# Optimization experiments

Measured on AMD Instinct MI355X. Metric: run time of the kernel, lower is better.

The kernel has to match this reference:

```python
import jax, jax.numpy as jnp
import numpy as np
import math

IN_C, OUT_C, KH, KW = 128, 128, 3, 3
GROUPS_NUM, NUM_W = 8, 8
STRIDE, PAD, DIL = 1, 1, 1
BETA = 1.0


def setup_inputs() -> dict:
    key = jax.random.key(0)
    ks = jax.random.split(key, 6)
    B, H, W = 8, 56, 56
    n = IN_C * KH * KW
    bound = math.sqrt(6.0 / n)  # reset_parameters bound for weight templates
    inputs = jax.random.normal(ks[0], (B, IN_C, H, W), jnp.float32)
    mask = jax.random.randint(ks[1], (B, H, W), 0, GROUPS_NUM)
    Alpha = jax.random.uniform(ks[2], (B, GROUPS_NUM, H, W), jnp.float32)
    weight_templates = jax.random.uniform(ks[3], (OUT_C * IN_C * KH * KW, NUM_W), jnp.float32, -bound, bound)
    routing_w = jax.random.normal(ks[4], (GROUPS_NUM * NUM_W, IN_C), jnp.float32) * 0.01
    routing_b = jnp.zeros((GROUPS_NUM * NUM_W,), jnp.float32)
    bias = jnp.zeros((OUT_C,), jnp.float32)
    return dict(inputs=inputs, mask=mask, Alpha=Alpha, weight_templates=weight_templates,
                routing_w=routing_w, routing_b=routing_b, bias=bias, use_alpha=1)


def _unfold(x):
    # torch F.unfold-compatible im2col: [B, C*KH*KW, Ho, Wo], channel-major feature order
    return jax.lax.conv_general_dilated_patches(
        x, (KH, KW), (STRIDE, STRIDE), [(PAD, PAD), (PAD, PAD)],
        rhs_dilation=(DIL, DIL), dimension_numbers=('NCHW', 'OIHW', 'NCHW'))


def reference(inputs, mask, Alpha, weight_templates, routing_w, routing_b, bias, use_alpha):
    B, C, H, W = inputs.shape
    K = IN_C * KH * KW
    # SE-style routing: GAP -> fc -> scaled sigmoid (alpha=1.0 in source)
    x_se = inputs.reshape(B, C, -1).mean(-1)                              # [B, C]
    x_se = 2.0 * jax.nn.sigmoid(x_se @ routing_w.T + routing_b) / NUM_W   # [B, G*num_W]
    # blend weight templates: F.linear(x_se.reshape(-1,num_W), weight)
    w = x_se.reshape(B * GROUPS_NUM, NUM_W) @ weight_templates.T          # [B*G, O*K]
    w = w.reshape(B, GROUPS_NUM, OUT_C, K).transpose(0, 2, 3, 1)          # [B, O, K, G]
    patches = _unfold(inputs)                                             # [B, K, Ho, Wo]
    # per-group convolution outputs, then per-pixel group routing
    y = jnp.einsum('bokg,bkhw->boghw', w, patches)                        # [B, O, G, Ho, Wo]
    if use_alpha:
        probs = jax.nn.softmax(BETA * Alpha, axis=1)                      # soft routing [B, G, Ho, Wo]
    else:
        probs = jax.nn.one_hot(mask, GROUPS_NUM, axis=1, dtype=y.dtype)   # hard per-pixel group select
    out = jnp.einsum('boghw,bghw->bohw', y, probs)
    return out + bias.reshape(1, -1, 1, 1)
```

## Files before the change

### kernel.cpp

```cpp
#include <hip/hip_runtime.h>
#include <stdint.h>

#define IN_C   128
#define OUT_C  128
#define KTOT   1152
#define NG     8
#define NW     8
#define NB     8
#define HH     56
#define WWID   56
#define NPIX   3136
#define PPAD   3200
#define MTOT   1024
#define HALO   58
#define HPIX   (HALO*HALO)


typedef __attribute__((ext_vector_type(8))) short short8;
typedef __attribute__((ext_vector_type(8))) unsigned short ushort8;
typedef __attribute__((ext_vector_type(4))) float f32x4;
typedef __attribute__((ext_vector_type(16))) float f32x16;

__device__ __forceinline__ unsigned short f2bf(float f) {
    unsigned u = __float_as_uint(f);
    u += 0x7FFF + ((u >> 16) & 1);
    return (unsigned short)(u >> 16);
}

__device__ __forceinline__ void cp16(const unsigned short* g, unsigned short* l) {
    __builtin_amdgcn_global_load_lds(
        (const __attribute__((address_space(1))) unsigned int*)g,
        (__attribute__((address_space(3))) unsigned int*)l,
        16, 0, 0);
}

__global__ __launch_bounds__(256) void prep_kernel(const float* __restrict__ in,
                                                   const float* __restrict__ T,
                                                   float* __restrict__ xse,
                                                   unsigned short* __restrict__ Apack,
                                                   unsigned short* __restrict__ Xt) {
    __shared__ __align__(16) unsigned char smem[32768];
    const int blk = blockIdx.x;
    const int t = threadIdx.x;

    if (blk < 1024) {
        const float* src = in + (size_t)blk * NPIX;
        float s = 0.f;
        for (int i = t; i < NPIX / 4; i += 256) {
            float4 v = ((const float4*)src)[i];
            s += v.x + v.y + v.z + v.w;
        }
        #pragma unroll
        for (int off = 32; off; off >>= 1) s += __shfl_down(s, off);
        float* ws4 = (float*)smem;
        if ((t & 63) == 0) ws4[t >> 6] = s;
        __syncthreads();
        if (t == 0)
            xse[blk] = (ws4[0] + ws4[1] + ws4[2] + ws4[3]) * (1.0f / (float)NPIX);
        return;
    }
    if (blk < 1152) {
        unsigned short* lh = (unsigned short*)smem;
        const int o = blk - 1024;
        const float* To = T + (size_t)o * 9216;
        #pragma unroll
        for (int it = 0; it < 9; it++) {
            const int f = it * 256 + t;
            const float4 v = ((const float4*)To)[f];
            ushort4 h;
            h.x = f2bf(v.x); h.y = f2bf(v.y); h.z = f2bf(v.z); h.w = f2bf(v.w);
            *(ushort4*)&lh[f * 4] = h;
        }
        __syncthreads();
        #pragma unroll
        for (int it = 0; it < 5; it++) {
            const int ch = it * 256 + t;
            if (ch < 1152) {
                const int j = ch & 7, kc = ch >> 3;
                const int s = kc >> 4, c0 = (kc & 15) << 3;
                const int stg = s * 4 + ((c0 >> 5) & 3);
                const int khb = (c0 >> 4) & 1;
                const int hib = (c0 >> 3) & 1;
                ushort8 v;
                #pragma unroll
                for (int i = 0; i < 8; i++)
                    v[i] = lh[((c0 + i) * 9 + s) * 8 + j];
                const size_t off = ((((size_t)(o >> 2) * 36 + stg) * 2 + khb) * 64
                                    + hib * 32 + (o & 3) * 8 + j) * 8;
                *(ushort8*)&Apack[off] = v;
            }
        }
        return;
    }
    unsigned short* tile = (unsigned short*)smem;
    const int idx = blk - 1152;
    const int yt = idx % 28;
    const int b  = idx / 28;
    const int y0 = yt * 2;

    #pragma unroll
    for (int it = 0; it < 14; it++) {
        const int f = it * 256 + t;
        const int c = f / 28;
        const int rem = f - c * 28;
        const int y = rem / 14;
        const int x4 = rem - y * 14;
        const float4 v = *(const float4*)(in + ((size_t)(b * IN_C + c)) * NPIX
                                          + (y0 + y) * WWID + x4 * 4);
        unsigned short bf0 = f2bf(v.x), bf1 = f2bf(v.y), bf2 = f2bf(v.z), bf3 = f2bf(v.w);
        const int ppb = (y * WWID + x4 * 4) ^ (((c >> 3) & 15) << 2);
        uint2 pk;
        pk.x = (unsigned)bf0 | ((unsigned)bf1 << 16);
        pk.y = (unsigned)bf2 | ((unsigned)bf3 << 16);
        *(uint2*)&tile[c * 128 + ppb] = pk;
    }
    __syncthreads();

    #pragma unroll
    for (int it = 0; it < 7; it++) {
        const int ch = it * 256 + t;
        const int oct = ch & 15;
        const int pp = ch >> 4;
        const int sw = oct << 2;
        ushort8 v;
        #pragma unroll
        for (int i = 0; i < 8; i++)
            v[i] = tile[(oct * 8 + i) * 128 + (pp ^ sw)];
        const int y2 = (pp >= WWID) ? 1 : 0;
        const int xg = pp - y2 * WWID;
        const size_t hp = (size_t)b * HPIX + (y0 + y2 + 1) * HALO + (xg + 1);
        *(ushort8*)&Xt[hp * 128 + oct * 8] = v;
    }

    if (t < 64) {
        const int pi = t >> 4, oct = t & 15;
        const int yy = y0 + 1 + (pi >> 1);
        const int xx = (pi & 1) * 57;
        *(ushort8*)&Xt[((size_t)b * HPIX + yy * HALO + xx) * 128 + oct * 8] =
            (ushort8){0, 0, 0, 0, 0, 0, 0, 0};
    }
    if (yt == 0 || yt == 27) {
        const int yy = (yt == 0) ? 0 : 57;
        #pragma unroll
        for (int it = 0; it < 4; it++) {
            const int ch = it * 256 + t;
            if (ch < 928) {
                const int xx = ch >> 4, oct = ch & 15;
                *(ushort8*)&Xt[((size_t)b * HPIX + yy * HALO + xx) * 128 + oct * 8] =
                    (ushort8){0, 0, 0, 0, 0, 0, 0, 0};
            }
        }
    }
}

__global__ __launch_bounds__(256) void s_kernel(const float* __restrict__ Alpha,
                                                const int* __restrict__ mask,
                                                const float* __restrict__ xse,
                                                const float* __restrict__ rw,
                                                const float* __restrict__ rb,
                                                const int* __restrict__ use_alpha,
                                                float* __restrict__ Sws) {
    const int b = blockIdx.y;
    const int t = threadIdx.x;
    const int p = blockIdx.x * 256 + t;
    __shared__ float xs[IN_C];
    __shared__ float rsh[64];
    if (t < IN_C) xs[t] = xse[b * IN_C + t];
    __syncthreads();
    if (t < 64) {
        float acc = rb[t];
        #pragma unroll 8
        for (int c = 0; c < IN_C; c++) acc += xs[c] * rw[t * IN_C + c];
        rsh[t] = 0.25f / (1.0f + expf(-acc));
    }
    __syncthreads();
    if (p >= PPAD) return;
    float sj[8] = {0, 0, 0, 0, 0, 0, 0, 0};
    if (p < NPIX) {
        float pr[8];
        if (use_alpha[0]) {
            float a[8], m = -1e30f;
            #pragma unroll
            for (int g = 0; g < 8; g++) {
                a[g] = Alpha[((size_t)(b * NG + g)) * NPIX + p];
                m = fmaxf(m, a[g]);
            }
            float sum = 0.f;
            #pragma unroll
            for (int g = 0; g < 8; g++) { pr[g] = expf(a[g] - m); sum += pr[g]; }
            float inv = 1.f / sum;
            #pragma unroll
            for (int g = 0; g < 8; g++) pr[g] *= inv;
        } else {
            int mg = mask[(size_t)b * NPIX + p];
            #pragma unroll
            for (int g = 0; g < 8; g++) pr[g] = (g == mg) ? 1.f : 0.f;
        }
        #pragma unroll
        for (int g = 0; g < 8; g++)
            #pragma unroll
            for (int j = 0; j < 8; j++) sj[j] += pr[g] * rsh[g * 8 + j];
    }
    float* dst = Sws + ((size_t)b * PPAD + p) * 8;
    *(f32x4*)dst = (f32x4){sj[0], sj[1], sj[2], sj[3]};
    *(f32x4*)(dst + 4) = (f32x4){sj[4], sj[5], sj[6], sj[7]};
}

__global__ __launch_bounds__(256) void gemm_kernel(const unsigned short* __restrict__ Apack,
                                                   const unsigned short* __restrict__ Xt,
                                                   const float* __restrict__ Sws,
                                                   const float* __restrict__ bias,
                                                   float* __restrict__ out) {
    __shared__ __align__(16) unsigned short Bsh[4][512 * 8];
    const int tid = threadIdx.x;
    const int wv = tid >> 6, ln = tid & 63;
    const int u  = ln & 31, hi = ln >> 5;
    const int wrow = wv >> 1, wcol = wv & 1;

    const int lid = blockIdx.x;
    const int b   = lid & 7;
    const int sl  = lid >> 3;
    const int mt  = sl & 7;
    const int nt  = sl >> 3;

    f32x16 acc[2][2];
    #pragma unroll
    for (int i = 0; i < 2; i++)
        #pragma unroll
        for (int j = 0; j < 2; j++)
            #pragma unroll
            for (int e = 0; e < 16; e++) acc[i][j][e] = 0.f;

    const int js = tid & 3;
    const int r0 = tid >> 2,  q0 = js ^ (r0 & 3) ^ ((r0 >> 2) & 3);
    const int r1 = r0 + 64,   q1 = js ^ (r1 & 3) ^ ((r1 >> 2) & 3);
    const int p0 = min(nt * 128 + r0, NPIX - 1);
    const int p1 = min(nt * 128 + r1, NPIX - 1);
    const int y0p = p0 / WWID, x0p = p0 - y0p * WWID;
    const int y1p = p1 / WWID, x1p = p1 - y1p * WWID;
    const unsigned short* gb0 = Xt + ((size_t)b * HPIX + y0p * HALO + x0p) * 128 + q0 * 8;
    const unsigned short* gb1 = Xt + ((size_t)b * HPIX + y1p * HALO + x1p) * 128 + q1 * 8;
    unsigned short* lbA[4];
    #pragma unroll
    for (int i = 0; i < 4; i++) lbA[i] = &Bsh[i][(wv * 64) * 8];

    const unsigned short* gawB[2];
    #pragma unroll
    for (int tm = 0; tm < 2; tm++) {
        const int m32 = mt * 4 + wrow * 2 + tm;
        gawB[tm] = Apack + (size_t)m32 * 36864 + ln * 8;
    }

    const int jbase = hi ^ (u & 3) ^ ((u >> 2) & 3);
    int boffL[2][2];
    #pragma unroll
    for (int tn = 0; tn < 2; tn++)
        #pragma unroll
        for (int kh = 0; kh < 2; kh++) {
            const int row = wcol * 64 + tn * 32 + u;
            boffL[tn][kh] = (row * 4 + (jbase ^ (kh << 1))) * 8;
        }

#define ALOAD(Ad, st_) { _Pragma("unroll")                                    \
        for (int tm_ = 0; tm_ < 2; tm_++) { _Pragma("unroll")                 \
            for (int kh_ = 0; kh_ < 2; kh_++)                                 \
                Ad[tm_][kh_] = *(const short8*)(gawB[tm_] + (st_) * 1024 + kh_ * 512); } }

#define STAGE(Ad, buf_) {                                                     \
        short8 b0 = *(const short8*)&Bsh[buf_][boffL[0][0]];                  \
        short8 b1 = *(const short8*)&Bsh[buf_][boffL[1][0]];                  \
        acc[0][0] = __builtin_amdgcn_mfma_f32_32x32x16_bf16(Ad[0][0], b0, acc[0][0], 0, 0, 0); \
        acc[0][1] = __builtin_amdgcn_mfma_f32_32x32x16_bf16(Ad[0][0], b1, acc[0][1], 0, 0, 0); \
        acc[1][0] = __builtin_amdgcn_mfma_f32_32x32x16_bf16(Ad[1][0], b0, acc[1][0], 0, 0, 0); \
        acc[1][1] = __builtin_amdgcn_mfma_f32_32x32x16_bf16(Ad[1][0], b1, acc[1][1], 0, 0, 0); \
        b0 = *(const short8*)&Bsh[buf_][boffL[0][1]];                         \
        b1 = *(const short8*)&Bsh[buf_][boffL[1][1]];                         \
        acc[0][0] = __builtin_amdgcn_mfma_f32_32x32x16_bf16(Ad[0][1], b0, acc[0][0], 0, 0, 0); \
        acc[0][1] = __builtin_amdgcn_mfma_f32_32x32x16_bf16(Ad[0][1], b1, acc[0][1], 0, 0, 0); \
        acc[1][0] = __builtin_amdgcn_mfma_f32_32x32x16_bf16(Ad[1][1], b0, acc[1][0], 0, 0, 0); \
        acc[1][1] = __builtin_amdgcn_mfma_f32_32x32x16_bf16(Ad[1][1], b1, acc[1][1], 0, 0, 0); }

    cp16(gb0, lbA[0]); cp16(gb1, lbA[0] + 256 * 8);
    cp16(gb0 + 32, lbA[1]); cp16(gb1 + 32, lbA[1] + 256 * 8);
    short8 A0[2][2], A1[2][2];
    ALOAD(A0, 0);
    ALOAD(A1, 1);

    #pragma unroll 1
    for (int pr = 0; pr < 18; pr++) {
        __syncthreads();
        const int st2 = pr * 2 + 2, st3 = pr * 2 + 3;
        if (pr < 17) {
            const int nk2 = st2 * 32, s2 = nk2 >> 7;
            const int kh2 = s2 / 3, kw2 = s2 - 3 * kh2;
            const int off2 = (kh2 * HALO + kw2) * 128 + (nk2 & 127);
            const int nk3 = st3 * 32, s3 = nk3 >> 7;
            const int kh3 = s3 / 3, kw3 = s3 - 3 * kh3;
            const int off3 = (kh3 * HALO + kw3) * 128 + (nk3 & 127);
            unsigned short* d2 = lbA[st2 & 3];
            unsigned short* d3 = lbA[st3 & 3];
            cp16(gb0 + off2, d2); cp16(gb1 + off2, d2 + 256 * 8);
            cp16(gb0 + off3, d3); cp16(gb1 + off3, d3 + 256 * 8);
        }
        const int bufa = (pr & 1) * 2;
        STAGE(A0, bufa);
        if (pr < 17) ALOAD(A0, st2);
        STAGE(A1, bufa + 1);
        if (pr < 17) ALOAD(A1, st3);
    }
#undef STAGE
#undef ALOAD

    const int j0 = hi * 4;
    #pragma unroll
    for (int tm = 0; tm < 2; tm++) {
        const int m32 = mt * 4 + wrow * 2 + tm;
        #pragma unroll
        for (int tn = 0; tn < 2; tn++) {
            const int p = nt * 128 + wcol * 64 + tn * 32 + u;
            const int pS = min(p, NPIX - 1);
            const f32x4 sv = *(const f32x4*)&Sws[((size_t)b * PPAD + pS) * 8 + j0];
            const f32x16 a = acc[tm][tn];
            #pragma unroll
            for (int q = 0; q < 4; q++) {
                float part = a[q * 4 + 0] * sv.x + a[q * 4 + 1] * sv.y
                           + a[q * 4 + 2] * sv.z + a[q * 4 + 3] * sv.w;
                float tot = part + __shfl_xor(part, 32);
                const int o = m32 * 4 + q;
                if (hi == 0 && p < NPIX)
                    out[((size_t)(b * OUT_C + o)) * NPIX + p] = tot + bias[o];
            }
        }
    }
}

extern "C" void kernel_launch(void* const* d_in, const int* in_sizes, int n_in,
                              void* d_out, int out_size, void* d_ws, size_t ws_size,
                              hipStream_t stream) {
    const float* inputs = (const float*)d_in[0];
    const int*   mask   = (const int*)d_in[1];
    const float* Alpha  = (const float*)d_in[2];
    const float* wtmpl  = (const float*)d_in[3];
    const float* rw     = (const float*)d_in[4];
    const float* rb     = (const float*)d_in[5];
    const float* bias   = (const float*)d_in[6];
    const int*   ua     = (const int*)d_in[7];
    float* out = (float*)d_out;

    char* ws = (char*)d_ws;
    unsigned short* Xt  = (unsigned short*)ws;
    unsigned short* Apk = (unsigned short*)(ws + 6889472);
    float*          Sws = (float*)(ws + 9248768);
    float*          xse = (float*)(ws + 10067968);

    prep_kernel<<<1376, 256, 0, stream>>>(inputs, wtmpl, xse, Apk, Xt);
    s_kernel<<<dim3(13, NB), 256, 0, stream>>>(Alpha, mask, xse, rw, rb, ua, Sws);
    gemm_kernel<<<1600, 256, 0, stream>>>(Apk, Xt, Sws, bias, out);
}
```

Before: 171.8 us.

## Double per-wave M tile in GEMM and relax the barrier's memory wait

Each wave now computes four 32-row output tiles instead of two, so each block covers 256 output channels per pixel tile and the grid shrinks from 1600 to 800 blocks. Each staged LDS B tile is reused across twice as many MFMAs, which halves the total im2col traffic from global memory to LDS. The full __syncthreads is replaced by s_waitcnt vmcnt(16) plus a raw barrier, so the in-flight A register prefetches are not drained at every step. The cost is higher register use (accumulators double to 128 floats) and fewer blocks to balance across CUs.

After: 193.0 us. 12.3% more time.

```diff
diff --git a/kernel.cpp b/kernel.cpp
--- a/kernel.cpp
+++ b/kernel.cpp
@@ -220,12 +220,12 @@
     const int lid = blockIdx.x;
     const int b   = lid & 7;
     const int sl  = lid >> 3;
-    const int mt  = sl & 7;
-    const int nt  = sl >> 3;
-
-    f32x16 acc[2][2];
-    #pragma unroll
-    for (int i = 0; i < 2; i++)
+    const int mt  = sl & 3;
+    const int nt  = sl >> 2;
+
+    f32x16 acc[4][2];
+    #pragma unroll
+    for (int i = 0; i < 4; i++)
         #pragma unroll
         for (int j = 0; j < 2; j++)
             #pragma unroll
@@ -244,12 +244,7 @@
     #pragma unroll
     for (int i = 0; i < 4; i++) lbA[i] = &Bsh[i][(wv * 64) * 8];
 
-    const unsigned short* gawB[2];
-    #pragma unroll
-    for (int tm = 0; tm < 2; tm++) {
-        const int m32 = mt * 4 + wrow * 2 + tm;
-        gawB[tm] = Apack + (size_t)m32 * 36864 + ln * 8;
-    }
+    const unsigned short* gA = Apack + (size_t)(mt * 8 + wrow * 4) * 36864 + ln * 8;
 
     const int jbase = hi ^ (u & 3) ^ ((u >> 2) & 3);
     int boffL[2][2];
@@ -262,33 +257,40 @@
         }
 
 #define ALOAD(Ad, st_) { _Pragma("unroll")                                    \
-        for (int tm_ = 0; tm_ < 2; tm_++) { _Pragma("unroll")                 \
+        for (int tm_ = 0; tm_ < 4; tm_++) { _Pragma("unroll")                 \
             for (int kh_ = 0; kh_ < 2; kh_++)                                 \
-                Ad[tm_][kh_] = *(const short8*)(gawB[tm_] + (st_) * 1024 + kh_ * 512); } }
+                Ad[tm_][kh_] = *(const short8*)(gA + (size_t)(st_) * 1024     \
+                                                + tm_ * 36864 + kh_ * 512); } }
 
 #define STAGE(Ad, buf_) {                                                     \
         short8 b0 = *(const short8*)&Bsh[buf_][boffL[0][0]];                  \
         short8 b1 = *(const short8*)&Bsh[buf_][boffL[1][0]];                  \
-        acc[0][0] = __builtin_amdgcn_mfma_f32_32x32x16_bf16(Ad[0][0], b0, acc[0][0], 0, 0, 0); \
-        acc[0][1] = __builtin_amdgcn_mfma_f32_32x32x16_bf16(Ad[0][0], b1, acc[0][1], 0, 0, 0); \
-        acc[1][0] = __builtin_amdgcn_mfma_f32_32x32x16_bf16(Ad[1][0], b0, acc[1][0], 0, 0, 0); \
-        acc[1][1] = __builtin_amdgcn_mfma_f32_32x32x16_bf16(Ad[1][0], b1, acc[1][1], 0, 0, 0); \
+        _Pragma("unroll")                                                     \
+        for (int tm_ = 0; tm_ < 4; tm_++) {                                   \
+            acc[tm_][0] = __builtin_amdgcn_mfma_f32_32x32x16_bf16(Ad[tm_][0], b0, acc[tm_][0], 0, 0, 0); \
+            acc[tm_][1] = __builtin_amdgcn_mfma_f32_32x32x16_bf16(Ad[tm_][0], b1, acc[tm_][1], 0, 0, 0); \
+        }                                                                     \
         b0 = *(const short8*)&Bsh[buf_][boffL[0][1]];                         \
         b1 = *(const short8*)&Bsh[buf_][boffL[1][1]];                         \
-        acc[0][0] = __builtin_amdgcn_mfma_f32_32x32x16_bf16(Ad[0][1], b0, acc[0][0], 0, 0, 0); \
-        acc[0][1] = __builtin_amdgcn_mfma_f32_32x32x16_bf16(Ad[0][1], b1, acc[0][1], 0, 0, 0); \
-        acc[1][0] = __builtin_amdgcn_mfma_f32_32x32x16_bf16(Ad[1][1], b0, acc[1][0], 0, 0, 0); \
-        acc[1][1] = __builtin_amdgcn_mfma_f32_32x32x16_bf16(Ad[1][1], b1, acc[1][1], 0, 0, 0); }
+        _Pragma("unroll")                                                     \
+        for (int tm_ = 0; tm_ < 4; tm_++) {                                   \
+            acc[tm_][0] = __builtin_amdgcn_mfma_f32_32x32x16_bf16(Ad[tm_][1], b0, acc[tm_][0], 0, 0, 0); \
+            acc[tm_][1] = __builtin_amdgcn_mfma_f32_32x32x16_bf16(Ad[tm_][1], b1, acc[tm_][1], 0, 0, 0); \
+        } }
 
     cp16(gb0, lbA[0]); cp16(gb1, lbA[0] + 256 * 8);
     cp16(gb0 + 32, lbA[1]); cp16(gb1 + 32, lbA[1] + 256 * 8);
-    short8 A0[2][2], A1[2][2];
+    short8 A0[4][2], A1[4][2];
     ALOAD(A0, 0);
     ALOAD(A1, 1);
 
     #pragma unroll 1
     for (int pr = 0; pr < 18; pr++) {
-        __syncthreads();
+        asm volatile("s_waitcnt vmcnt(16)" ::: "memory");
+        __builtin_amdgcn_sched_barrier(0);
+        __builtin_amdgcn_s_barrier();
+        __builtin_amdgcn_sched_barrier(0);
+
         const int st2 = pr * 2 + 2, st3 = pr * 2 + 3;
         if (pr < 17) {
             const int nk2 = st2 * 32, s2 = nk2 >> 7;
@@ -313,8 +315,8 @@
 
     const int j0 = hi * 4;
     #pragma unroll
-    for (int tm = 0; tm < 2; tm++) {
-        const int m32 = mt * 4 + wrow * 2 + tm;
+    for (int tm = 0; tm < 4; tm++) {
+        const int m32 = mt * 8 + wrow * 4 + tm;
         #pragma unroll
         for (int tn = 0; tn < 2; tn++) {
             const int p = nt * 128 + wcol * 64 + tn * 32 + u;
@@ -355,5 +357,5 @@
 
     prep_kernel<<<1376, 256, 0, stream>>>(inputs, wtmpl, xse, Apk, Xt);
     s_kernel<<<dim3(13, NB), 256, 0, stream>>>(Alpha, mask, xse, rw, rb, ua, Sws);
-    gemm_kernel<<<1600, 256, 0, stream>>>(Apk, Xt, Sws, bias, out);
-}
+    gemm_kernel<<<800, 256, 0, stream>>>(Apk, Xt, Sws, bias, out);
+}
```
